# Kernel tuning notes

Hardware: AMD Instinct MI355X
Metric: run time of the kernel (lower is better)

The kernel has to match this reference:

```python
import jax, jax.numpy as jnp
import numpy as np

STRIDE = 1  # module init arg


def setup_inputs() -> dict:
    key = jax.random.key(0)
    k1, k2 = jax.random.split(key)
    x = jax.random.normal(k1, (16, 32, 256, 256), dtype=jnp.float32)
    kernel = jax.random.normal(k2, (32, 5, 5), dtype=jnp.float32) * 0.1
    return {"input": x, "kernel": kernel}


def _maxmin_conv(x, kernel, stride=STRIDE):
    # Max-min semifield convolution:
    #   out[b,oc,i,j] = max_{c,dy,dx} min(x_pad[b,c,i*s+dy,j*s+dx], k[oc,dy,dx])
    # Since min(., k) is monotone in x, the max over in-channels commutes:
    #   max_{c} min(x_c, k) == min(max_c x_c, k)
    # so we reduce channels once up front (same math, far less memory).
    K = kernel.shape[-1]
    p = K - 1
    top = p // 2
    bot = p - top  # calculate_padding(): left=top=floor(p/2), right=bottom=p-top
    xmax = jnp.max(x, axis=1)  # [B, H, W]
    xp = jnp.pad(xmax, ((0, 0), (top, bot), (top, bot)), constant_values=-np.inf)
    B, Hp, Wp = xp.shape
    Ho = (Hp - K) // stride + 1
    Wo = (Wp - K) // stride + 1
    OC = kernel.shape[0]
    acc = jnp.full((B, OC, Ho, Wo), -np.inf, dtype=x.dtype)
    for dy in range(K):  # fixed small K*K loop over kernel taps
        for dx in range(K):
            patch = xp[:, dy:dy + stride * Ho:stride, dx:dx + stride * Wo:stride]  # [B,Ho,Wo]
            cand = jnp.minimum(patch[:, None, :, :], kernel[None, :, dy, dx, None, None])
            acc = jnp.maximum(acc, cand)
    return acc


def reference(input, kernel):
    return _maxmin_conv(input, kernel)
```

## Files before the change

kernel.cpp:

```cpp
#include <hip/hip_runtime.h>
#include <math.h>


#define BATCH 16
#define CH    32
#define OCH   32
#define HH    256
#define WW    256
#define HWSZ  (HH * WW)
#define TW    32
#define TH    16
#define LH    20
#define LW    42
#define NWG   (BATCH * (HH / (2 * TH)) * (WW / TW))

typedef float floatx4 __attribute__((ext_vector_type(4)));

__device__ __forceinline__ float vmax3(float a, float b, float c) {
    float d;
    asm("v_max3_f32 %0, %1, %2, %3" : "=v"(d) : "v"(a), "v"(b), "v"(c));
    return d;
}

__device__ __forceinline__ void conv_oc(const float (&w)[6][8], const float* __restrict__ kk,
                                        int oc, float* __restrict__ out, size_t obq) {
    const float* kw = kk + oc * 25;
    float kr[25];
#pragma unroll
    for (int i = 0; i < 25; ++i) kr[i] = kw[i];
#pragma unroll
    for (int r = 0; r < 2; ++r) {
        float a[4];
#pragma unroll
        for (int j = 0; j < 4; ++j) {
            float mm[25];
#pragma unroll
            for (int dy = 0; dy < 5; ++dy)
#pragma unroll
                for (int dx = 0; dx < 5; ++dx)
                    mm[dy * 5 + dx] = fminf(w[r + dy][j + dx], kr[dy * 5 + dx]);
            float t0 = vmax3(mm[0],  mm[1],  mm[2]);
            float t1 = vmax3(mm[3],  mm[4],  mm[5]);
            float t2 = vmax3(mm[6],  mm[7],  mm[8]);
            float t3 = vmax3(mm[9],  mm[10], mm[11]);
            float t4 = vmax3(mm[12], mm[13], mm[14]);
            float t5 = vmax3(mm[15], mm[16], mm[17]);
            float t6 = vmax3(mm[18], mm[19], mm[20]);
            float t7 = vmax3(mm[21], mm[22], mm[23]);
            a[j] = vmax3(vmax3(t0, t1, t2), vmax3(t3, t4, t5), vmax3(t6, t7, mm[24]));
        }
        floatx4 ov = { a[0], a[1], a[2], a[3] };
        __builtin_nontemporal_store(ov, (floatx4*)(out + obq + (size_t)r * WW));
    }
}

__global__ __launch_bounds__(256, 2) void fused_maxmin_kernel(const float* __restrict__ x,
                                                              const float* __restrict__ kk,
                                                              float* __restrict__ out) {
    __shared__ float xmt[2][LH][LW];
    int tid = threadIdx.x;
    int bid = blockIdx.x;
    int swz = (bid & 7) * (NWG >> 3) + (bid >> 3);
    int b   = swz >> 6;
    int t2  = swz & 63;
    int ty2 = t2 >> 3;
    int tx  = t2 & 7;

    const float NI = -INFINITY;

    int pr = tid / 10, pc = tid % 10;
    int c4 = tx * 8 - 1 + pc;
    bool cvalid = (c4 >= 0) && (c4 < WW / 4);
    int c4c = c4 < 0 ? 0 : (c4 > WW / 4 - 1 ? WW / 4 - 1 : c4);
    const float4* xb4 = (const float4*)x + (size_t)b * CH * (HWSZ / 4);

    if (tid < 200) {
        int rw = ty2 * 32 - 2 + pr;
        bool valid = cvalid && (rw >= 0) && (rw < HH);
        int rwc = rw < 0 ? 0 : (rw > HH - 1 ? HH - 1 : rw);
        const float4* src = xb4 + (size_t)rwc * (WW / 4) + c4c;
        float4 m = src[0];
#pragma unroll
        for (int c = 1; c < CH; ++c) {
            float4 v = src[(size_t)c * (HWSZ / 4)];
            m.x = fmaxf(m.x, v.x); m.y = fmaxf(m.y, v.y);
            m.z = fmaxf(m.z, v.z); m.w = fmaxf(m.w, v.w);
        }
        if (!valid) { m.x = NI; m.y = NI; m.z = NI; m.w = NI; }
        *(float2*)&xmt[0][pr][4 * pc]     = make_float2(m.x, m.y);
        *(float2*)&xmt[0][pr][4 * pc + 2] = make_float2(m.z, m.w);
    }
    __syncthreads();

    int xg = tid & 7;
    int rg = (tid >> 3) & 7;
    int wv = __builtin_amdgcn_readfirstlane(tid >> 6);

    int rw1 = ty2 * 32 + 14 + pr;
    bool valid1 = cvalid && (rw1 < HH);
    int rwc1 = rw1 > HH - 1 ? HH - 1 : rw1;
    const float4* src1 = xb4 + (size_t)rwc1 * (WW / 4) + c4c;

    float w[6][8];
#pragma unroll
    for (int r = 0; r < 6; ++r) {
        const float* rp = &xmt[0][2 * rg + r][4 * xg + 2];
#pragma unroll
        for (int s = 0; s < 4; ++s)
            *(float2*)&w[r][2 * s] = *(const float2*)(rp + 2 * s);
    }

    size_t ob0 = (size_t)(b * OCH + wv * 8) * HWSZ
               + (size_t)(ty2 * 32 + 2 * rg) * WW + tx * TW + 4 * xg;

    float4 macc = make_float4(NI, NI, NI, NI);
    bool act = tid < 200;
#pragma unroll
    for (int o = 0; o < 8; ++o) {
        float4 v0, v1, v2, v3;
        if (act) {
            v0 = src1[(size_t)(4 * o + 0) * (HWSZ / 4)];
            v1 = src1[(size_t)(4 * o + 1) * (HWSZ / 4)];
            v2 = src1[(size_t)(4 * o + 2) * (HWSZ / 4)];
            v3 = src1[(size_t)(4 * o + 3) * (HWSZ / 4)];
        }
        conv_oc(w, kk, wv * 8 + o, out, ob0 + (size_t)o * HWSZ);
        if (act) {
            macc.x = fmaxf(macc.x, fmaxf(fmaxf(v0.x, v1.x), fmaxf(v2.x, v3.x)));
            macc.y = fmaxf(macc.y, fmaxf(fmaxf(v0.y, v1.y), fmaxf(v2.y, v3.y)));
            macc.z = fmaxf(macc.z, fmaxf(fmaxf(v0.z, v1.z), fmaxf(v2.z, v3.z)));
            macc.w = fmaxf(macc.w, fmaxf(fmaxf(v0.w, v1.w), fmaxf(v2.w, v3.w)));
        }
    }
    if (act) {
        if (!valid1) { macc.x = NI; macc.y = NI; macc.z = NI; macc.w = NI; }
        *(float2*)&xmt[1][pr][4 * pc]     = make_float2(macc.x, macc.y);
        *(float2*)&xmt[1][pr][4 * pc + 2] = make_float2(macc.z, macc.w);
    }
    __syncthreads();

#pragma unroll
    for (int r = 0; r < 6; ++r) {
        const float* rp = &xmt[1][2 * rg + r][4 * xg + 2];
#pragma unroll
        for (int s = 0; s < 4; ++s)
            *(float2*)&w[r][2 * s] = *(const float2*)(rp + 2 * s);
    }
    size_t ob1 = ob0 + (size_t)16 * WW;
#pragma unroll
    for (int o = 0; o < 8; ++o)
        conv_oc(w, kk, wv * 8 + o, out, ob1 + (size_t)o * HWSZ);
}

extern "C" void kernel_launch(void* const* d_in, const int* in_sizes, int n_in,
                              void* d_out, int out_size, void* d_ws, size_t ws_size,
                              hipStream_t stream) {
    const float* x  = (const float*)d_in[0];
    const float* kk = (const float*)d_in[1];
    float* out      = (float*)d_out;
    fused_maxmin_kernel<<<NWG, 256, 0, stream>>>(x, kk, out);
}
```

Baseline: 58.43 us.

## Double-buffer second-half channel loads and relax barriers to LDS-only waits

Second-half channel-max loads are now issued one group ahead into a two-slot register buffer, so global latency overlaps the conv compute of the previous output channel. __syncthreads is replaced by an lgkmcnt-only wait plus s_barrier, which avoids draining outstanding global stores. Launch bounds rise to 4 waves per SIMD and the second conv loop is no longer unrolled, both aimed at cutting register use for higher occupancy. This risks spills or a slower rolled loop, and the bare barrier depends on correct waitcnt semantics.

```diff
diff --git a/kernel.cpp b/kernel.cpp
--- a/kernel.cpp
+++ b/kernel.cpp
@@ -8,11 +8,9 @@
 #define HH    256
 #define WW    256
 #define HWSZ  (HH * WW)
-#define TW    32
-#define TH    16
 #define LH    20
 #define LW    42
-#define NWG   (BATCH * (HH / (2 * TH)) * (WW / TW))
+#define NWG   (BATCH * (HH / 32) * (WW / 32))
 
 typedef float floatx4 __attribute__((ext_vector_type(4)));
 
@@ -20,6 +18,11 @@
     float d;
     asm("v_max3_f32 %0, %1, %2, %3" : "=v"(d) : "v"(a), "v"(b), "v"(c));
     return d;
+}
+
+__device__ __forceinline__ void lgkm_barrier() {
+    asm volatile("s_waitcnt lgkmcnt(0)" ::: "memory");
+    __builtin_amdgcn_s_barrier();
 }
 
 __device__ __forceinline__ void conv_oc(const float (&w)[6][8], const float* __restrict__ kk,
@@ -54,7 +57,7 @@
     }
 }
 
-__global__ __launch_bounds__(256, 2) void fused_maxmin_kernel(const float* __restrict__ x,
+__global__ __launch_bounds__(256, 4) void fused_maxmin_kernel(const float* __restrict__ x,
                                                               const float* __restrict__ kk,
                                                               float* __restrict__ out) {
     __shared__ float xmt[2][LH][LW];
@@ -73,8 +76,9 @@
     bool cvalid = (c4 >= 0) && (c4 < WW / 4);
     int c4c = c4 < 0 ? 0 : (c4 > WW / 4 - 1 ? WW / 4 - 1 : c4);
     const float4* xb4 = (const float4*)x + (size_t)b * CH * (HWSZ / 4);
+    bool act = tid < 200;
 
-    if (tid < 200) {
+    if (act) {
         int rw = ty2 * 32 - 2 + pr;
         bool valid = cvalid && (rw >= 0) && (rw < HH);
         int rwc = rw < 0 ? 0 : (rw > HH - 1 ? HH - 1 : rw);
@@ -90,7 +94,7 @@
         *(float2*)&xmt[0][pr][4 * pc]     = make_float2(m.x, m.y);
         *(float2*)&xmt[0][pr][4 * pc + 2] = make_float2(m.z, m.w);
     }
-    __syncthreads();
+    lgkm_barrier();
 
     int xg = tid & 7;
     int rg = (tid >> 3) & 7;
@@ -100,6 +104,12 @@
     bool valid1 = cvalid && (rw1 < HH);
     int rwc1 = rw1 > HH - 1 ? HH - 1 : rw1;
     const float4* src1 = xb4 + (size_t)rwc1 * (WW / 4) + c4c;
+
+    float4 v[2][4];
+    if (act) {
+#pragma unroll
+        for (int j = 0; j < 4; ++j) v[0][j] = src1[(size_t)j * (HWSZ / 4)];
+    }
 
     float w[6][8];
 #pragma unroll
@@ -111,33 +121,31 @@
     }
 
     size_t ob0 = (size_t)(b * OCH + wv * 8) * HWSZ
-               + (size_t)(ty2 * 32 + 2 * rg) * WW + tx * TW + 4 * xg;
+               + (size_t)(ty2 * 32 + 2 * rg) * WW + tx * 32 + 4 * xg;
 
     float4 macc = make_float4(NI, NI, NI, NI);
-    bool act = tid < 200;
 #pragma unroll
     for (int o = 0; o < 8; ++o) {
-        float4 v0, v1, v2, v3;
+        if (o < 7 && act) {
+#pragma unroll
+            for (int j = 0; j < 4; ++j)
+                v[(o + 1) & 1][j] = src1[(size_t)(4 * (o + 1) + j) * (HWSZ / 4)];
+        }
         if (act) {
-            v0 = src1[(size_t)(4 * o + 0) * (HWSZ / 4)];
-            v1 = src1[(size_t)(4 * o + 1) * (HWSZ / 4)];
-            v2 = src1[(size_t)(4 * o + 2) * (HWSZ / 4)];
-            v3 = src1[(size_t)(4 * o + 3) * (HWSZ / 4)];
+            const float4* c = v[o & 1];
+            macc.x = fmaxf(macc.x, fmaxf(fmaxf(c[0].x, c[1].x), fmaxf(c[2].x, c[3].x)));
+            macc.y = fmaxf(macc.y, fmaxf(fmaxf(c[0].y, c[1].y), fmaxf(c[2].y, c[3].y)));
+            macc.z = fmaxf(macc.z, fmaxf(fmaxf(c[0].z, c[1].z), fmaxf(c[2].z, c[3].z)));
+            macc.w = fmaxf(macc.w, fmaxf(fmaxf(c[0].w, c[1].w), fmaxf(c[2].w, c[3].w)));
         }
         conv_oc(w, kk, wv * 8 + o, out, ob0 + (size_t)o * HWSZ);
-        if (act) {
-            macc.x = fmaxf(macc.x, fmaxf(fmaxf(v0.x, v1.x), fmaxf(v2.x, v3.x)));
-            macc.y = fmaxf(macc.y, fmaxf(fmaxf(v0.y, v1.y), fmaxf(v2.y, v3.y)));
-            macc.z = fmaxf(macc.z, fmaxf(fmaxf(v0.z, v1.z), fmaxf(v2.z, v3.z)));
-            macc.w = fmaxf(macc.w, fmaxf(fmaxf(v0.w, v1.w), fmaxf(v2.w, v3.w)));
-        }
     }
     if (act) {
         if (!valid1) { macc.x = NI; macc.y = NI; macc.z = NI; macc.w = NI; }
         *(float2*)&xmt[1][pr][4 * pc]     = make_float2(macc.x, macc.y);
         *(float2*)&xmt[1][pr][4 * pc + 2] = make_float2(macc.z, macc.w);
     }
-    __syncthreads();
+    lgkm_barrier();
 
 #pragma unroll
     for (int r = 0; r < 6; ++r) {
@@ -147,7 +155,6 @@
             *(float2*)&w[r][2 * s] = *(const float2*)(rp + 2 * s);
     }
     size_t ob1 = ob0 + (size_t)16 * WW;
-#pragma unroll
     for (int o = 0; o < 8; ++o)
         conv_oc(w, kk, wv * 8 + o, out, ob1 + (size_t)o * HWSZ);
 }
```

After: 109.1 us. +86.6%, slower.
